# Performance work log

Measured on AMD Instinct MI355X. Metric: run time of the kernel, lower is better.

Reference implementation:

```python
import jax, jax.numpy as jnp
import numpy as np

B, C, H, W = 16, 64, 128, 128
C8 = C // 8

def setup_inputs() -> dict:
    key = jax.random.key(0)
    ks = jax.random.split(key, 9)
    s = 0.05
    return {
        "x": jax.random.normal(ks[0], (B, C, H, W), jnp.float32),
        "y": jax.random.normal(ks[1], (B, C, H, W), jnp.float32),
        "query_w": jax.random.normal(ks[2], (C8, C), jnp.float32) * s,
        "query_b": jax.random.normal(ks[3], (C8,), jnp.float32) * s,
        "key_w": jax.random.normal(ks[4], (C8, C), jnp.float32) * s,
        "key_b": jax.random.normal(ks[5], (C8,), jnp.float32) * s,
        "value_w": jax.random.normal(ks[6], (C, 2 * C), jnp.float32) * s,
        "value_b": jax.random.normal(ks[7], (C,), jnp.float32) * s,
        "gamma": jax.random.normal(ks[8], (), jnp.float32) * 0.1,
    }

def _conv1x1(t, w, b):
    # t: [B, Cin, H, W], w: [Cout, Cin] -> [B, Cout, H, W]
    return jnp.einsum('oc,bchw->bohw', w, t) + b[None, :, None, None]

def reference(x, y, query_w, query_b, key_w, key_b, value_w, value_b, gamma):
    b, c, h, w = x.shape
    q = _conv1x1(x, query_w, query_b)                       # [B, C8, H, W]
    k = _conv1x1(y, key_w, key_b)                           # [B, C8, H, W]
    v = _conv1x1(jnp.concatenate([x, y], axis=1), value_w, value_b)  # [B, C, H, W]

    # axial energies: H-axis (g indexes key rows), W-axis (u indexes key cols)
    energy_H = jnp.einsum('bchw,bcgw->bhwg', q, k)          # [B, H, W, H]
    energy_W = jnp.einsum('bchw,bchu->bhwu', q, k)          # [B, H, W, W]

    # -inf on the H diagonal (self position counted once, via the W branch)
    eye = jnp.eye(h, dtype=bool)                            # [H, H]
    energy_H = jnp.where(eye[None, :, None, :], -jnp.inf, energy_H)

    att = jax.nn.softmax(jnp.concatenate([energy_H, energy_W], axis=3), axis=3)
    att_H = att[..., :h]                                    # [B, H, W, H]
    att_W = att[..., h:]                                    # [B, H, W, W]

    out_H = jnp.einsum('bcgw,bhwg->bchw', v, att_H)
    out_W = jnp.einsum('bchu,bhwu->bchw', v, att_W)
    return gamma * (out_H + out_W) + x + y
```

## Files before the change

### kernel.cpp

```cpp
#include <hip/hip_runtime.h>

#define NCH 80
#define HW 16384

typedef unsigned short u16;
typedef unsigned int u32;
typedef short s16x8 __attribute__((ext_vector_type(8)));
typedef float f32x4 __attribute__((ext_vector_type(4)));

__device__ __forceinline__ float b2f_lo(u32 pk){ union{u32 u; float f;} c; c.u = pk<<16; return c.f; }
__device__ __forceinline__ float b2f_hi(u32 pk){ union{u32 u; float f;} c; c.u = pk & 0xffff0000u; return c.f; }
__device__ __forceinline__ float b2f(u16 v){ union{u32 u; float f;} c; c.u = ((u32)v)<<16; return c.f; }
__device__ __forceinline__ u16 f2b_hw(float f){
    union{ __bf16 h; u16 s; } c; c.h = (__bf16)f; return c.s;
}
__device__ __forceinline__ u32 pk2(float a, float b){
    return (u32)f2b_hw(a) | ((u32)f2b_hw(b)<<16);
}
#define NEG_INF (-__builtin_inff())

union U4S8 { uint4 u; s16x8 v; };

__global__ __launch_bounds__(256) void k_wcvt(
    const float* __restrict__ qw, const float* __restrict__ qb,
    const float* __restrict__ kw, const float* __restrict__ kb,
    const float* __restrict__ vw, const float* __restrict__ vb,
    u16* __restrict__ wbf, float* __restrict__ bias80)
{
    int i = blockIdx.x*256 + threadIdx.x;
    int ch = i >> 7, cin = i & 127;
    float v;
    if (ch < 8)       v = (cin < 64) ? qw[ch*64 + cin] : 0.f;
    else if (ch < 16) v = (cin >= 64) ? kw[(ch-8)*64 + (cin-64)] : 0.f;
    else              v = vw[(ch-16)*128 + cin];
    wbf[i] = f2b_hw(v);
    if (i < 80){
        bias80[i] = (i<8) ? qb[i] : (i<16) ? kb[i-8] : vb[i-16];
    }
}

__global__ __launch_bounds__(256) void k_qkv_mfma(
    const float* __restrict__ x, const float* __restrict__ y,
    const u16* __restrict__ wbf, const float* __restrict__ bias80,
    u16* __restrict__ qkv, u16* __restrict__ xy)
{
    __shared__ u32 a32[64*132];

    int t = threadIdx.x;
    int p0 = blockIdx.x * 128;
    int b = p0 >> 14, rem = p0 & 16383;
    const float* xb = x + (size_t)b*64*HW + rem;
    const float* yb = y + (size_t)b*64*HW + rem;

    float4 fx0[4], fx1[4], fy0[4], fy1[4];
    #pragma unroll
    for (int r=0;r<4;r++){
        int idx = t + r*256;
        int cp = idx >> 5;
        int pxg = (idx & 31) * 4;
        const float* xp = xb + (size_t)(2*cp)*HW + pxg;
        const float* yp = yb + (size_t)(2*cp)*HW + pxg;
        fx0[r] = *(const float4*)xp;
        fx1[r] = *(const float4*)(xp + HW);
        fy0[r] = *(const float4*)yp;
        fy1[r] = *(const float4*)(yp + HW);
    }
    #pragma unroll
    for (int r=0;r<4;r++){
        int idx = t + r*256;
        int cp = idx >> 5;
        int pxg = (idx & 31) * 4;
        uint4 wx, wy;
        wx.x = pk2(fx0[r].x, fx1[r].x);
        wx.y = pk2(fx0[r].y, fx1[r].y);
        wx.z = pk2(fx0[r].z, fx1[r].z);
        wx.w = pk2(fx0[r].w, fx1[r].w);
        wy.x = pk2(fy0[r].x, fy1[r].x);
        wy.y = pk2(fy0[r].y, fy1[r].y);
        wy.z = pk2(fy0[r].z, fy1[r].z);
        wy.w = pk2(fy0[r].w, fy1[r].w);
        *(uint4*)&a32[cp*132 + pxg]       = wx;
        *(uint4*)&a32[(32+cp)*132 + pxg]  = wy;
        if (xy){
            uint2 s0, s1;
            s0.x = pk2(fx0[r].x+fy0[r].x, fx0[r].y+fy0[r].y);
            s0.y = pk2(fx0[r].z+fy0[r].z, fx0[r].w+fy0[r].w);
            s1.x = pk2(fx1[r].x+fy1[r].x, fx1[r].y+fy1[r].y);
            s1.y = pk2(fx1[r].z+fy1[r].z, fx1[r].w+fy1[r].w);
            *(uint2*)&xy[(size_t)(b*64 + 2*cp)*HW + rem + pxg]     = s0;
            *(uint2*)&xy[(size_t)(b*64 + 2*cp+1)*HW + rem + pxg]   = s1;
        }
    }
    __syncthreads();

    int wv = t >> 6, l = t & 63;
    int lm = l & 15, lq = l >> 4;

    s16x8 af[2][4];
    #pragma unroll
    for (int m2=0;m2<2;m2++){
        int pxl = (wv*2 + m2)*16 + lm;
        #pragma unroll
        for (int ks=0;ks<4;ks++){
            int cpb = (ks&1)*16 + lq*4 + ((ks>>1)*32);
            U4S8 uu;
            uu.u = make_uint4(a32[(cpb+0)*132 + pxl], a32[(cpb+1)*132 + pxl],
                              a32[(cpb+2)*132 + pxl], a32[(cpb+3)*132 + pxl]);
            af[m2][ks] = uu.v;
        }
    }

    #pragma unroll
    for (int nt=0;nt<5;nt++){
        int ch = nt*16 + lm;
        const u16* wrow = wbf + ch*128 + lq*8;
        s16x8 b0 = *(const s16x8*)(wrow);
        s16x8 b1 = *(const s16x8*)(wrow + 32);
        s16x8 b2 = *(const s16x8*)(wrow + 64);
        s16x8 b3 = *(const s16x8*)(wrow + 96);
        f32x4 acc0 = (f32x4){0.f,0.f,0.f,0.f};
        f32x4 acc1 = (f32x4){0.f,0.f,0.f,0.f};
        acc0 = __builtin_amdgcn_mfma_f32_16x16x32_bf16(af[0][0], b0, acc0, 0,0,0);
        acc1 = __builtin_amdgcn_mfma_f32_16x16x32_bf16(af[1][0], b0, acc1, 0,0,0);
        acc0 = __builtin_amdgcn_mfma_f32_16x16x32_bf16(af[0][1], b1, acc0, 0,0,0);
        acc1 = __builtin_amdgcn_mfma_f32_16x16x32_bf16(af[1][1], b1, acc1, 0,0,0);
        acc0 = __builtin_amdgcn_mfma_f32_16x16x32_bf16(af[0][2], b2, acc0, 0,0,0);
        acc1 = __builtin_amdgcn_mfma_f32_16x16x32_bf16(af[1][2], b2, acc1, 0,0,0);
        acc0 = __builtin_amdgcn_mfma_f32_16x16x32_bf16(af[0][3], b3, acc0, 0,0,0);
        acc1 = __builtin_amdgcn_mfma_f32_16x16x32_bf16(af[1][3], b3, acc1, 0,0,0);
        float bs = bias80[ch];
        size_t chbase = (size_t)(b*NCH + ch)*HW + rem;
        uint2 st0, st1;
        st0.x = pk2(acc0[0]+bs, acc0[1]+bs);
        st0.y = pk2(acc0[2]+bs, acc0[3]+bs);
        st1.x = pk2(acc1[0]+bs, acc1[1]+bs);
        st1.y = pk2(acc1[2]+bs, acc1[3]+bs);
        *(uint2*)&qkv[chbase + (wv*2+0)*16 + lq*4] = st0;
        *(uint2*)&qkv[chbase + (wv*2+1)*16 + lq*4] = st1;
    }
}

__global__ __launch_bounds__(256) void k_tr(const u16* __restrict__ src, u16* __restrict__ dst)
{
    __shared__ u16 tile[64][65];
    int blk = blockIdx.x;
    int plane = blk >> 2, tq = blk & 3;
    int r0 = (tq >> 1) * 64, c0 = (tq & 1) * 64;
    const u16* s = src + (size_t)plane * HW;
    u16* d = dst + (size_t)plane * HW;
    int col = threadIdx.x & 63, rr = threadIdx.x >> 6;
    #pragma unroll
    for (int k=0;k<16;k++){
        int r = k*4 + rr;
        tile[r][col] = s[(r0+r)*128 + c0 + col];
    }
    __syncthreads();
    #pragma unroll
    for (int k=0;k<16;k++){
        int r = k*4 + rr;
        d[(c0+r)*128 + r0 + col] = tile[col][r];
    }
}

__global__ __launch_bounds__(512, 4) void k_col(
    const u16* __restrict__ qkvT, u16* __restrict__ colT,
    float* __restrict__ mH, float* __restrict__ sH)
{
    __shared__ __align__(16) float q_s[8*128];
    __shared__ __align__(16) float k_sw[8*128];
    __shared__ __align__(16) u16  v_bf[64*128];
    __shared__ __align__(16) u16  p_bf[128*128];

    int t = threadIdx.x;
    int b = blockIdx.x >> 7, w = blockIdx.x & 127;
    const u32* src = (const u32*)(qkvT + (size_t)b*NCH*HW + w*128);
    u32* v32 = (u32*)v_bf;
    u32* p32 = (u32*)p_bf;

    #pragma unroll
    for (int r=0;r<2;r++){
        int idx = t + r*512;
        int ch = idx >> 6, hp = idx & 63;
        u32 pk = src[ch*8192 + hp];
        int g0 = hp*2;
        if (ch < 8){
            *(float2*)&q_s[ch*128 + g0] = make_float2(b2f_lo(pk), b2f_hi(pk));
        } else {
            int o = ch - 8;
            k_sw[g0*8     + (o ^ ((g0>>3)&7))]     = b2f_lo(pk);
            k_sw[(g0+1)*8 + (o ^ (((g0+1)>>3)&7))] = b2f_hi(pk);
        }
    }
    #pragma unroll
    for (int r=0;r<8;r++){
        int idx = t + r*512;
        int c = idx >> 6, gp = idx & 63;
        v32[(c*64 + gp) ^ ((c&7)<<2)] = src[(16+c)*8192 + gp];
    }
    __syncthreads();

    int tr = t >> 4, tc = t & 15;
    int h0 = tr*4, g0 = tc*8;
    float e[4][8];
    #pragma unroll
    for (int i=0;i<4;i++)
        #pragma unroll
        for (int j=0;j<8;j++) e[i][j] = 0.f;

    #pragma unroll
    for (int o=0;o<8;o++){
        float qv[4], kv[8];
        #pragma unroll
        for (int i=0;i<4;i++) qv[i] = q_s[o*128 + h0 + i];
        int kb = o ^ (tc & 7);
        #pragma unroll
        for (int j=0;j<8;j++) kv[j] = k_sw[(g0+j)*8 + kb];
        #pragma unroll
        for (int i=0;i<4;i++)
            #pragma unroll
            for (int j=0;j<8;j++) e[i][j] += qv[i]*kv[j];
    }
    #pragma unroll
    for (int i=0;i<4;i++){
        int h = h0 + i;
        if ((h>>3) == tc) e[i][h&7] = NEG_INF;
    }
    #pragma unroll
    for (int i=0;i<4;i++){
        int h = h0 + i;
        float m = e[i][0];
        #pragma unroll
        for (int j=1;j<8;j++) m = fmaxf(m, e[i][j]);
        m = fmaxf(m, __shfl_xor(m,1));
        m = fmaxf(m, __shfl_xor(m,2));
        m = fmaxf(m, __shfl_xor(m,4));
        m = fmaxf(m, __shfl_xor(m,8));
        float s = 0.f;
        #pragma unroll
        for (int j=0;j<8;j++){ float pp = __expf(e[i][j]-m); e[i][j]=pp; s += pp; }
        s += __shfl_xor(s,1);
        s += __shfl_xor(s,2);
        s += __shfl_xor(s,4);
        s += __shfl_xor(s,8);
        if (tc == 0){
            mH[b*HW + h*128 + w] = m;
            sH[b*HW + h*128 + w] = s;
        }
        uint4 pw;
        pw.x = pk2(e[i][0], e[i][1]);
        pw.y = pk2(e[i][2], e[i][3]);
        pw.z = pk2(e[i][4], e[i][5]);
        pw.w = pk2(e[i][6], e[i][7]);
        *(uint4*)&p32[(h*64 + tc*4) ^ ((h&7)<<2)] = pw;
    }
    __syncthreads();

    int wv = t >> 6, l = t & 63;
    int lm = l & 15, lq = l >> 4;
    int mt = wv;
    f32x4 acc[4];
    #pragma unroll
    for (int nt=0; nt<4; nt++) acc[nt] = (f32x4){0.f,0.f,0.f,0.f};

    #pragma unroll
    for (int ks=0; ks<4; ks++){
        int ri = mt*16 + lm;
        s16x8 a = *(const s16x8*)&p32[(ri*64 + ks*16 + lq*4) ^ ((ri&7)<<2)];
        #pragma unroll
        for (int nt=0; nt<4; nt++){
            int c = nt*16 + lm;
            s16x8 bf_ = *(const s16x8*)&v32[(c*64 + ks*16 + lq*4) ^ ((c&7)<<2)];
            acc[nt] = __builtin_amdgcn_mfma_f32_16x16x32_bf16(a, bf_, acc[nt], 0, 0, 0);
        }
    }
    #pragma unroll
    for (int nt=0; nt<4; nt++){
        int c = nt*16 + lm;
        int hh = mt*16 + lq*4;
        uint2 st;
        st.x = pk2(acc[nt][0], acc[nt][1]);
        st.y = pk2(acc[nt][2], acc[nt][3]);
        *(uint2*)&colT[((size_t)(b*64+c)*128 + w)*128 + hh] = st;
    }
}

__global__ __launch_bounds__(512, 4) void k_row(
    const u16* __restrict__ qkv, const u16* __restrict__ colpart,
    const float* __restrict__ mH, const float* __restrict__ sH,
    const float* __restrict__ x, const float* __restrict__ y,
    const u16* __restrict__ xy,
    const float* __restrict__ gamma_p, float* __restrict__ out)
{
    __shared__ __align__(16) float q_s[8*128];
    __shared__ __align__(16) float k_sw[8*128];
    __shared__ __align__(16) u16  v_bf[64*128];
    __shared__ __align__(16) u16  p_bf[128*128];
    __shared__ float fc_s[128], fr_s[128];

    int t = threadIdx.x;
    int b = blockIdx.x >> 7, h = blockIdx.x & 127;
    const u32* src = (const u32*)(qkv + (size_t)b*NCH*HW + h*128);
    u32* v32 = (u32*)v_bf;
    u32* p32 = (u32*)p_bf;

    #pragma unroll
    for (int r=0;r<2;r++){
        int idx = t + r*512;
        int ch = idx >> 6, wp = idx & 63;
        u32 pk = src[ch*8192 + wp];
        int u0 = wp*2;
        if (ch < 8){
            *(float2*)&q_s[ch*128 + u0] = make_float2(b2f_lo(pk), b2f_hi(pk));
        } else {
            int o = ch - 8;
            k_sw[u0*8     + (o ^ ((u0>>3)&7))]     = b2f_lo(pk);
            k_sw[(u0+1)*8 + (o ^ (((u0+1)>>3)&7))] = b2f_hi(pk);
        }
    }
    #pragma unroll
    for (int r=0;r<8;r++){
        int idx = t + r*512;
        int c = idx >> 6, up = idx & 63;
        v32[(c*64 + up) ^ ((c&7)<<2)] = src[(16+c)*8192 + up];
    }
    __syncthreads();

    int tr = t >> 4, tc = t & 15;
    int w0 = tr*4, u0 = tc*8;
    float e[4][8];
    #pragma unroll
    for (int i=0;i<4;i++)
        #pragma unroll
        for (int j=0;j<8;j++) e[i][j] = 0.f;

    #pragma unroll
    for (int o=0;o<8;o++){
        float qv[4], kv[8];
        #pragma unroll
        for (int i=0;i<4;i++) qv[i] = q_s[o*128 + w0 + i];
        int kb = o ^ (tc & 7);
        #pragma unroll
        for (int j=0;j<8;j++) kv[j] = k_sw[(u0+j)*8 + kb];
        #pragma unroll
        for (int i=0;i<4;i++)
            #pragma unroll
            for (int j=0;j<8;j++) e[i][j] += qv[i]*kv[j];
    }
    int pixbase = b*HW + h*128;
    #pragma unroll
    for (int i=0;i<4;i++){
        int wp = w0 + i;
        float m = e[i][0];
        #pragma unroll
        for (int j=1;j<8;j++) m = fmaxf(m, e[i][j]);
        m = fmaxf(m, __shfl_xor(m,1));
        m = fmaxf(m, __shfl_xor(m,2));
        m = fmaxf(m, __shfl_xor(m,4));
        m = fmaxf(m, __shfl_xor(m,8));
        float mh = mH[pixbase + wp];
        float sh = sH[pixbase + wp];
        float mg = fmaxf(m, mh);
        float s = 0.f;
        #pragma unroll
        for (int j=0;j<8;j++){ float pp = __expf(e[i][j]-mg); e[i][j]=pp; s += pp; }
        s += __shfl_xor(s,1);
        s += __shfl_xor(s,2);
        s += __shfl_xor(s,4);
        s += __shfl_xor(s,8);
        if (tc == 0){
            float ef = __expf(mh - mg);
            float stot = sh*ef + s;
            fc_s[wp] = ef/stot;
            fr_s[wp] = 1.0f/stot;
        }
        uint4 pw;
        pw.x = pk2(e[i][0], e[i][1]);
        pw.y = pk2(e[i][2], e[i][3]);
        pw.z = pk2(e[i][4], e[i][5]);
        pw.w = pk2(e[i][6], e[i][7]);
        *(uint4*)&p32[(wp*64 + tc*4) ^ ((wp&7)<<2)] = pw;
    }
    __syncthreads();

    int wv = t >> 6, l = t & 63;
    int lm = l & 15, lq = l >> 4;
    int mt = wv;
    f32x4 acc[4];
    #pragma unroll
    for (int nt=0; nt<4; nt++) acc[nt] = (f32x4){0.f,0.f,0.f,0.f};

    #pragma unroll
    for (int ks=0; ks<4; ks++){
        int ri = mt*16 + lm;
        s16x8 a = *(const s16x8*)&p32[(ri*64 + ks*16 + lq*4) ^ ((ri&7)<<2)];
        #pragma unroll
        for (int nt=0; nt<4; nt++){
            int c = nt*16 + lm;
            s16x8 bf_ = *(const s16x8*)&v32[(c*64 + ks*16 + lq*4) ^ ((c&7)<<2)];
            acc[nt] = __builtin_amdgcn_mfma_f32_16x16x32_bf16(a, bf_, acc[nt], 0, 0, 0);
        }
    }
    float gm = gamma_p[0];
    int wq0 = mt*16 + lq*4;
    float fcv[4], frv[4];
    #pragma unroll
    for (int r2=0;r2<4;r2++){ fcv[r2] = fc_s[wq0+r2]; frv[r2] = fr_s[wq0+r2]; }

    #pragma unroll
    for (int nt=0; nt<4; nt++){
        int c = nt*16 + lm;
        size_t off = ((size_t)(b*64+c)*128 + h)*128 + wq0;
        uint2 cpv = *(const uint2*)&colpart[off];
        float cp[4] = {b2f_lo(cpv.x), b2f_hi(cpv.x), b2f_lo(cpv.y), b2f_hi(cpv.y)};
        float xs[4];
        if (xy){
            uint2 xv = *(const uint2*)&xy[off];
            xs[0]=b2f_lo(xv.x); xs[1]=b2f_hi(xv.x); xs[2]=b2f_lo(xv.y); xs[3]=b2f_hi(xv.y);
        } else {
            float4 x4 = *(const float4*)&x[off];
            float4 y4 = *(const float4*)&y[off];
            xs[0]=x4.x+y4.x; xs[1]=x4.y+y4.y; xs[2]=x4.z+y4.z; xs[3]=x4.w+y4.w;
        }
        float4 o4;
        o4.x = gm*(cp[0]*fcv[0] + acc[nt][0]*frv[0]) + xs[0];
        o4.y = gm*(cp[1]*fcv[1] + acc[nt][1]*frv[1]) + xs[1];
        o4.z = gm*(cp[2]*fcv[2] + acc[nt][2]*frv[2]) + xs[2];
        o4.w = gm*(cp[3]*fcv[3] + acc[nt][3]*frv[3]) + xs[3];
        *(float4*)&out[off] = o4;
    }
}

extern "C" void kernel_launch(void* const* d_in, const int* in_sizes, int n_in,
                              void* d_out, int out_size, void* d_ws, size_t ws_size,
                              hipStream_t stream)
{
    (void)in_sizes; (void)n_in; (void)out_size;
    const float* x  = (const float*)d_in[0];
    const float* y  = (const float*)d_in[1];
    const float* qw = (const float*)d_in[2];
    const float* qb = (const float*)d_in[3];
    const float* kw = (const float*)d_in[4];
    const float* kb = (const float*)d_in[5];
    const float* vw = (const float*)d_in[6];
    const float* vb = (const float*)d_in[7];
    const float* gm = (const float*)d_in[8];
    float* out = (float*)d_out;

    char* ws = (char*)d_ws;
    u16* qkv     = (u16*)(ws);
    u16* qkvT    = (u16*)(ws + 41943040ull);
    u16* colT    = (u16*)(ws + 83886080ull);
    u16* colpart = qkvT;
    float* mH    = (float*)(ws + 117440512ull);
    float* sH    = (float*)(ws + 118489088ull);
    u16* wbf     = (u16*)(ws + 119537664ull);
    float* bias80= (float*)(ws + 119558144ull);
    u16* xybuf   = nullptr;
    if (ws_size >= 119603200ull + 33554432ull)
        xybuf = (u16*)(ws + 119603200ull);

    k_wcvt<<<40, 256, 0, stream>>>(qw, qb, kw, kb, vw, vb, wbf, bias80);
    k_qkv_mfma<<<2048, 256, 0, stream>>>(x, y, wbf, bias80, qkv, xybuf);
    k_tr <<<5120, 256, 0, stream>>>(qkv, qkvT);
    k_col<<<2048, 512, 0, stream>>>(qkvT, colT, mH, sH);
    k_tr <<<4096, 256, 0, stream>>>(colT, colpart);
    k_row<<<2048, 512, 0, stream>>>(qkv, colpart, mH, sH, x, y, xybuf, gm, out);
}
```

Baseline: 165.5 us.

## Write column output directly in row layout and remap blocks for XCD locality

k_col now writes its bf16 results straight into the [b,c,h,w] layout that k_row consumes, so the separate transpose kernel and its extra round trip through memory are gone. The block index is also remapped so that neighbouring w columns of the same batch go to the same XCD, which aims to make the scattered 2-byte stores merge in that XCD's L2. The cost is uncoalesced scalar 16-bit stores strided by 256 bytes in place of packed 8-byte stores.

```diff
diff --git a/kernel.cpp b/kernel.cpp
--- a/kernel.cpp
+++ b/kernel.cpp
@@ -10,7 +10,6 @@
 
 __device__ __forceinline__ float b2f_lo(u32 pk){ union{u32 u; float f;} c; c.u = pk<<16; return c.f; }
 __device__ __forceinline__ float b2f_hi(u32 pk){ union{u32 u; float f;} c; c.u = pk & 0xffff0000u; return c.f; }
-__device__ __forceinline__ float b2f(u16 v){ union{u32 u; float f;} c; c.u = ((u32)v)<<16; return c.f; }
 __device__ __forceinline__ u16 f2b_hw(float f){
     union{ __bf16 h; u16 s; } c; c.h = (__bf16)f; return c.s;
 }
@@ -163,7 +162,7 @@
 }
 
 __global__ __launch_bounds__(512, 4) void k_col(
-    const u16* __restrict__ qkvT, u16* __restrict__ colT,
+    const u16* __restrict__ qkvT, u16* __restrict__ colp,
     float* __restrict__ mH, float* __restrict__ sH)
 {
     __shared__ __align__(16) float q_s[8*128];
@@ -172,7 +171,12 @@
     __shared__ __align__(16) u16  p_bf[128*128];
 
     int t = threadIdx.x;
-    int b = blockIdx.x >> 7, w = blockIdx.x & 127;
+    int i = blockIdx.x;
+    int xcd = i & 7, n = i >> 3;
+    int chunk = (n >> 5)*8 + xcd;
+    int b = chunk >> 2;
+    int w = ((chunk & 3) << 5) + (n & 31);
+
     const u32* src = (const u32*)(qkvT + (size_t)b*NCH*HW + w*128);
     u32* v32 = (u32*)v_bf;
     u32* p32 = (u32*)p_bf;
@@ -203,41 +207,41 @@
     int h0 = tr*4, g0 = tc*8;
     float e[4][8];
     #pragma unroll
-    for (int i=0;i<4;i++)
-        #pragma unroll
-        for (int j=0;j<8;j++) e[i][j] = 0.f;
+    for (int i2=0;i2<4;i2++)
+        #pragma unroll
+        for (int j=0;j<8;j++) e[i2][j] = 0.f;
 
     #pragma unroll
     for (int o=0;o<8;o++){
         float qv[4], kv[8];
         #pragma unroll
-        for (int i=0;i<4;i++) qv[i] = q_s[o*128 + h0 + i];
+        for (int i2=0;i2<4;i2++) qv[i2] = q_s[o*128 + h0 + i2];
         int kb = o ^ (tc & 7);
         #pragma unroll
         for (int j=0;j<8;j++) kv[j] = k_sw[(g0+j)*8 + kb];
         #pragma unroll
-        for (int i=0;i<4;i++)
+        for (int i2=0;i2<4;i2++)
             #pragma unroll
-            for (int j=0;j<8;j++) e[i][j] += qv[i]*kv[j];
-    }
-    #pragma unroll
-    for (int i=0;i<4;i++){
-        int h = h0 + i;
-        if ((h>>3) == tc) e[i][h&7] = NEG_INF;
-    }
-    #pragma unroll
-    for (int i=0;i<4;i++){
-        int h = h0 + i;
-        float m = e[i][0];
-        #pragma unroll
-        for (int j=1;j<8;j++) m = fmaxf(m, e[i][j]);
+            for (int j=0;j<8;j++) e[i2][j] += qv[i2]*kv[j];
+    }
+    #pragma unroll
+    for (int i2=0;i2<4;i2++){
+        int h = h0 + i2;
+        if ((h>>3) == tc) e[i2][h&7] = NEG_INF;
+    }
+    #pragma unroll
+    for (int i2=0;i2<4;i2++){
+        int h = h0 + i2;
+        float m = e[i2][0];
+        #pragma unroll
+        for (int j=1;j<8;j++) m = fmaxf(m, e[i2][j]);
         m = fmaxf(m, __shfl_xor(m,1));
         m = fmaxf(m, __shfl_xor(m,2));
         m = fmaxf(m, __shfl_xor(m,4));
         m = fmaxf(m, __shfl_xor(m,8));
         float s = 0.f;
         #pragma unroll
-        for (int j=0;j<8;j++){ float pp = __expf(e[i][j]-m); e[i][j]=pp; s += pp; }
+        for (int j=0;j<8;j++){ float pp = __expf(e[i2][j]-m); e[i2][j]=pp; s += pp; }
         s += __shfl_xor(s,1);
         s += __shfl_xor(s,2);
         s += __shfl_xor(s,4);
@@ -247,10 +251,10 @@
             sH[b*HW + h*128 + w] = s;
         }
         uint4 pw;
-        pw.x = pk2(e[i][0], e[i][1]);
-        pw.y = pk2(e[i][2], e[i][3]);
-        pw.z = pk2(e[i][4], e[i][5]);
-        pw.w = pk2(e[i][6], e[i][7]);
+        pw.x = pk2(e[i2][0], e[i2][1]);
+        pw.y = pk2(e[i2][2], e[i2][3]);
+        pw.z = pk2(e[i2][4], e[i2][5]);
+        pw.w = pk2(e[i2][6], e[i2][7]);
         *(uint4*)&p32[(h*64 + tc*4) ^ ((h&7)<<2)] = pw;
     }
     __syncthreads();
@@ -276,11 +280,12 @@
     #pragma unroll
     for (int nt=0; nt<4; nt++){
         int c = nt*16 + lm;
+        size_t base = (size_t)(b*64+c)*HW + w;
         int hh = mt*16 + lq*4;
-        uint2 st;
-        st.x = pk2(acc[nt][0], acc[nt][1]);
-        st.y = pk2(acc[nt][2], acc[nt][3]);
-        *(uint2*)&colT[((size_t)(b*64+c)*128 + w)*128 + hh] = st;
+        colp[base + (size_t)(hh+0)*128] = f2b_hw(acc[nt][0]);
+        colp[base + (size_t)(hh+1)*128] = f2b_hw(acc[nt][1]);
+        colp[base + (size_t)(hh+2)*128] = f2b_hw(acc[nt][2]);
+        colp[base + (size_t)(hh+3)*128] = f2b_hw(acc[nt][3]);
     }
 }
 
@@ -449,8 +454,7 @@
     char* ws = (char*)d_ws;
     u16* qkv     = (u16*)(ws);
     u16* qkvT    = (u16*)(ws + 41943040ull);
-    u16* colT    = (u16*)(ws + 83886080ull);
-    u16* colpart = qkvT;
+    u16* colpart = (u16*)(ws + 83886080ull);
     float* mH    = (float*)(ws + 117440512ull);
     float* sH    = (float*)(ws + 118489088ull);
     u16* wbf     = (u16*)(ws + 119537664ull);
@@ -462,7 +466,6 @@
     k_wcvt<<<40, 256, 0, stream>>>(qw, qb, kw, kb, vw, vb, wbf, bias80);
     k_qkv_mfma<<<2048, 256, 0, stream>>>(x, y, wbf, bias80, qkv, xybuf);
     k_tr <<<5120, 256, 0, stream>>>(qkv, qkvT);
-    k_col<<<2048, 512, 0, stream>>>(qkvT, colT, mH, sH);
-    k_tr <<<4096, 256, 0, stream>>>(colT, colpart);
+    k_col<<<2048, 512, 0, stream>>>(qkvT, colpart, mH, sH);
     k_row<<<2048, 512, 0, stream>>>(qkv, colpart, mH, sH, x, y, xybuf, gm, out);
 }
```

Result: slower. 206.9 us (+25.0%).
